# Optimization experiments

Hardware: AMD Instinct MI355X
Metric: run time of the kernel (lower is better)

## Reference

```python
import jax, jax.numpy as jnp
import numpy as np

H = 8
D_MODEL = 1024
D_K = D_MODEL // H
NEG = -1000000000.0


def layer_norm(x, a, b, eps=1e-06):
    # torch std: unbiased (ddof=1); module divides by (std + eps)
    mean = jnp.mean(x, axis=-1, keepdims=True)
    var = jnp.sum((x - mean) ** 2, axis=-1, keepdims=True) / (x.shape[-1] - 1)
    std = jnp.sqrt(var)
    return a * (x - mean) / (std + eps) + b


def setup_inputs() -> dict:
    key = jax.random.key(0)
    ks = jax.random.split(key, 12)
    B, S, D = 8, 1024, D_MODEL
    inp = {
        "query": jax.random.normal(ks[0], (B, S, D), jnp.float32),
        "value": jax.random.normal(ks[1], (B, S, D), jnp.float32),
        "key": jax.random.normal(ks[2], (B, S, D), jnp.float32),
        "mask": jax.random.randint(ks[3], (B, S), 0, 2, jnp.int32),
        "ln_a": jnp.ones((D,), jnp.float32),
        "ln_b": jnp.zeros((D,), jnp.float32),
        "wq": jax.random.normal(ks[4], (D, D), jnp.float32) * 0.02,
        "bq": jnp.zeros((D,), jnp.float32),
        "wk": jax.random.normal(ks[5], (D, D), jnp.float32) * 0.02,
        "bk": jnp.zeros((D,), jnp.float32),
        "wv": jax.random.normal(ks[6], (D, D), jnp.float32) * 0.02,
        "bv": jnp.zeros((D,), jnp.float32),
        "w_aoa": jax.random.normal(ks[7], (2 * D, 2 * D), jnp.float32) * 0.02,  # [out, in]
        "b_aoa": jnp.zeros((2 * D,), jnp.float32),
    }
    return inp


def reference(query, value, key, mask, ln_a, ln_b, wq, bq, wk, bk, wv, bv, w_aoa, b_aoa):
    B, S, D = query.shape
    # mask [B,S] -> [B,1,1,S]
    m = mask[:, None, None, :]
    # norm_q
    q = layer_norm(query, ln_a, ln_b)
    # QKV projections, split heads -> [B,H,S,Dk]
    def split_heads(x):
        return x.reshape(B, -1, H, D_K).transpose(0, 2, 1, 3)
    q_ = split_heads(q @ wq.T + bq)
    k_ = split_heads(key @ wk.T + bk)
    v_ = split_heads(value @ wv.T + bv)
    scores = jnp.einsum("bhqd,bhkd->bhqk", q_, k_) / jnp.sqrt(jnp.float32(D_K))
    scores = jnp.where(m == 0, NEG, scores)
    p = jax.nn.softmax(scores, axis=-1)
    x = jnp.einsum("bhqk,bhkd->bhqd", p, v_)
    x = x.transpose(0, 2, 1, 3).reshape(B, S, D)
    # AoA: concat with (normed) query, linear to 2D, GLU
    z = jnp.concatenate([x, q], axis=-1) @ w_aoa.T + b_aoa
    a, g = jnp.split(z, 2, axis=-1)
    return a * jax.nn.sigmoid(g)
```

## Files before the change

kernel.cpp:

```cpp
#include <hip/hip_runtime.h>

typedef __attribute__((ext_vector_type(8))) __bf16 bf16x8;
typedef __attribute__((ext_vector_type(4))) float f32x4;
typedef __attribute__((ext_vector_type(16))) float f32x16;
typedef __attribute__((ext_vector_type(2))) int i32x2;

__device__ __forceinline__ ushort f2b(float f) {
    uint u = __builtin_bit_cast(uint, f);
    u += 0x7fffu + ((u >> 16) & 1u);
    return (ushort)(u >> 16);
}
__device__ __forceinline__ float b2f(ushort h) {
    uint u = ((uint)h) << 16;
    return __builtin_bit_cast(float, u);
}
__device__ __forceinline__ uint cvtpk(float a, float b) {
    uint r;
    asm("v_cvt_pk_bf16_f32 %0, %1, %2" : "=v"(r) : "v"(a), "v"(b));
    return r;
}

__global__ __launch_bounds__(256) void cast_all(const float* __restrict__ wq,
                                                const float* __restrict__ wk,
                                                const float* __restrict__ wv,
                                                const float* __restrict__ waoa,
                                                ushort* __restrict__ wqb,
                                                ushort* __restrict__ wab) {
    int bid = blockIdx.x;
    int tid = threadIdx.x;
    if (bid < 3072) {
        const float* src = (bid < 1024) ? wq : ((bid < 2048) ? wk : wv);
        float4 v = *(const float4*)(src + ((size_t)(bid & 1023) * 256 + tid) * 4);
        ushort4 o;
        o.x = f2b(v.x); o.y = f2b(v.y); o.z = f2b(v.z); o.w = f2b(v.w);
        *(ushort4*)(wqb + (size_t)bid * 1024 + tid * 4) = o;
    } else {
        int b3 = bid - 3072;
        int n1 = b3 >> 1;
        int c = (b3 & 1) * 1024 + tid * 4;
        int q = ((n1 & 63) | ((n1 >> 7) << 6)) + ((n1 >> 6) & 1) * 1024;
        float4 v = *(const float4*)(waoa + (size_t)q * 2048 + c);
        ushort4 o;
        o.x = f2b(v.x); o.y = f2b(v.y); o.z = f2b(v.z); o.w = f2b(v.w);
        *(ushort4*)(wab + (size_t)n1 * 2048 + c) = o;
    }
}

__global__ __launch_bounds__(256) void ln_kernel(const float* __restrict__ x,
                                                 const float* __restrict__ ga,
                                                 const float* __restrict__ be,
                                                 ushort* __restrict__ xq) {
    const int row = blockIdx.x, tid = threadIdx.x;
    __shared__ float red[4];
    float4 v = ((const float4*)(x + (size_t)row * 1024))[tid];
    float sm = v.x + v.y + v.z + v.w;
    for (int off = 32; off; off >>= 1) sm += __shfl_xor(sm, off);
    if ((tid & 63) == 0) red[tid >> 6] = sm;
    __syncthreads();
    float mean = (red[0] + red[1] + red[2] + red[3]) * (1.f / 1024.f);
    __syncthreads();
    float dx = v.x - mean, dy = v.y - mean, dz = v.z - mean, dw = v.w - mean;
    float s2 = dx * dx + dy * dy + dz * dz + dw * dw;
    for (int off = 32; off; off >>= 1) s2 += __shfl_xor(s2, off);
    if ((tid & 63) == 0) red[tid >> 6] = s2;
    __syncthreads();
    float var = (red[0] + red[1] + red[2] + red[3]) * (1.f / 1023.f);
    float inv = 1.f / (sqrtf(var) + 1e-6f);
    float4 g = ((const float4*)ga)[tid];
    float4 bb = ((const float4*)be)[tid];
    ushort4 o;
    o.x = f2b(g.x * dx * inv + bb.x);
    o.y = f2b(g.y * dy * inv + bb.y);
    o.z = f2b(g.z * dz * inv + bb.z);
    o.w = f2b(g.w * dw * inv + bb.w);
    *(ushort4*)&xq[(size_t)row * 2048 + 1024 + tid * 4] = o;
}

template <int MODE>
__global__ __launch_bounds__(512, 2) void gemm6(const ushort* __restrict__ Aq, int ldaq,
                                                const ushort* __restrict__ B, int ldb,
                                                const float* __restrict__ bias0,
                                                void* __restrict__ out0,
                                                int K, int NB) {
    __shared__ ushort lds[2][32768];

    const int tid = threadIdx.x;
    const int w = tid >> 6, l = tid & 63;
    const int wr = w >> 2, wcn = w & 3;
    const int r16 = l & 15, g4 = l >> 4;

    const int bid = blockIdx.x;
    const int cpx = gridDim.x >> 3;
    const int swz = (bid & 7) * cpx + (bid >> 3);
    const int m0 = (swz / NB) * 256;
    const int n0 = (swz % NB) * 256;

    const ushort* A = Aq;
    const int lda = ldaq;

    const int srow8 = l >> 3;
    const int sxor8 = ((l & 7) ^ srow8) * 8;
    const ushort* As0 = A + (size_t)(m0 + w * 8 + srow8) * lda + sxor8;
    const ushort* Bs0 = B + (size_t)(n0 + w * 8 + srow8) * ldb + sxor8;

    f32x4 acc[8][4];
#pragma unroll
    for (int i = 0; i < 8; i++)
#pragma unroll
        for (int j = 0; j < 4; j++) acc[i][j] = (f32x4){0.f, 0.f, 0.f, 0.f};

    const int sw16 = (r16 & 7) << 4;
    char* ldsb = (char*)&lds[0][0];

#define STAGE_H(sel_, HS_, kt_)                                                            \
    do {                                                                                   \
        const int mat_ = (HS_)&1, half_ = (HS_) >> 1;                                      \
        const ushort* sb_ = mat_ ? Bs0 : As0;                                              \
        const int ld_ = mat_ ? ldb : lda;                                                  \
        _Pragma("unroll") for (int li_ = 0; li_ < 2; li_++) {                              \
            const ushort* src_ = sb_ + (size_t)(half_ * 128 + li_ * 64) * ld_ + (kt_)*64;  \
            int dst_ = (sel_)*65536 + mat_ * 32768 + half_ * 16384 + li_ * 8192 + w * 1024;\
            __builtin_amdgcn_global_load_lds(                                              \
                (const __attribute__((address_space(1))) void*)src_,                       \
                (__attribute__((address_space(3))) void*)(ldsb + dst_), 16, 0, 0);         \
        }                                                                                  \
    } while (0)

    auto LDA4 = [&](bf16x8 (&dst)[4][2], int sel, int half) {
#pragma unroll
        for (int ai = 0; ai < 4; ai++)
#pragma unroll
            for (int ks = 0; ks < 2; ks++)
                dst[ai][ks] = *(const bf16x8*)(ldsb + sel * 65536 + half * 16384 +
                                               (wr * 16 + 32 * ai + r16) * 128 +
                                               ((ks * 64 + g4 * 16) ^ sw16));
    };
    auto LDB2 = [&](bf16x8 (&dst)[2][2], int sel, int half) {
#pragma unroll
        for (int bi = 0; bi < 2; bi++)
#pragma unroll
            for (int ks = 0; ks < 2; ks++)
                dst[bi][ks] = *(const bf16x8*)(ldsb + sel * 65536 + 32768 + half * 16384 +
                                               (wcn * 16 + 64 * bi + r16) * 128 +
                                               ((ks * 64 + g4 * 16) ^ sw16));
    };
    auto MM = [&](bf16x8 (&af)[4][2], bf16x8 (&bf)[2][2], int A0, int B0) {
        __builtin_amdgcn_s_setprio(1);
#pragma unroll
        for (int ks = 0; ks < 2; ks++)
#pragma unroll
            for (int ai = 0; ai < 4; ai++)
#pragma unroll
                for (int bi = 0; bi < 2; bi++)
                    acc[A0 + ai][B0 + bi] = __builtin_amdgcn_mfma_f32_16x16x32_bf16(
                        af[ai][ks], bf[bi][ks], acc[A0 + ai][B0 + bi], 0, 0, 0);
        __builtin_amdgcn_s_setprio(0);
    };

    const int NT = K >> 6;

    STAGE_H(0, 0, 0); STAGE_H(0, 1, 0); STAGE_H(0, 2, 0); STAGE_H(0, 3, 0);
    STAGE_H(1, 0, 1); STAGE_H(1, 1, 1); STAGE_H(1, 2, 1);
    asm volatile("s_waitcnt vmcnt(10)" ::: "memory");
    __builtin_amdgcn_s_barrier();

    bf16x8 aL[4][2], aH[4][2], bL[2][2], bH[2][2];

    for (int t = 0; t < NT - 2; ++t) {
        const int sel = t & 1;
        LDA4(aL, sel, 0); LDB2(bL, sel, 0);
        STAGE_H(sel ^ 1, 3, t + 1);
        __builtin_amdgcn_s_barrier();
        MM(aL, bL, 0, 0);
        asm volatile("s_waitcnt vmcnt(10)" ::: "memory");
        __builtin_amdgcn_s_barrier();
        LDA4(aH, sel, 1);
        STAGE_H(sel, 0, t + 2);
        __builtin_amdgcn_s_barrier();
        MM(aH, bL, 4, 0);
        asm volatile("s_waitcnt vmcnt(10)" ::: "memory");
        __builtin_amdgcn_s_barrier();
        LDB2(bH, sel, 1);
        STAGE_H(sel, 1, t + 2);
        __builtin_amdgcn_s_barrier();
        MM(aH, bH, 4, 2);
        __builtin_amdgcn_s_barrier();
        STAGE_H(sel, 2, t + 2);
        __builtin_amdgcn_s_barrier();
        MM(aL, bH, 0, 2);
        asm volatile("s_waitcnt vmcnt(10)" ::: "memory");
        __builtin_amdgcn_s_barrier();
    }
    {
        const int sel = (NT - 2) & 1;
        LDA4(aL, sel, 0); LDB2(bL, sel, 0);
        STAGE_H(sel ^ 1, 3, NT - 1);
        __builtin_amdgcn_s_barrier();
        MM(aL, bL, 0, 0);
        asm volatile("s_waitcnt vmcnt(10)" ::: "memory");
        __builtin_amdgcn_s_barrier();
        LDA4(aH, sel, 1);
        __builtin_amdgcn_s_barrier();
        MM(aH, bL, 4, 0);
        asm volatile("s_waitcnt vmcnt(8)" ::: "memory");
        __builtin_amdgcn_s_barrier();
        LDB2(bH, sel, 1);
        __builtin_amdgcn_s_barrier();
        MM(aH, bH, 4, 2);
        __builtin_amdgcn_s_barrier();
        MM(aL, bH, 0, 2);
        asm volatile("s_waitcnt vmcnt(4)" ::: "memory");
        __builtin_amdgcn_s_barrier();
    }
    {
        const int sel = (NT - 1) & 1;
        LDA4(aL, sel, 0); LDB2(bL, sel, 0);
        __builtin_amdgcn_s_barrier();
        MM(aL, bL, 0, 0);
        asm volatile("s_waitcnt vmcnt(2)" ::: "memory");
        __builtin_amdgcn_s_barrier();
        LDA4(aH, sel, 1);
        __builtin_amdgcn_s_barrier();
        MM(aH, bL, 4, 0);
        asm volatile("s_waitcnt vmcnt(0)" ::: "memory");
        __builtin_amdgcn_s_barrier();
        LDB2(bH, sel, 1);
        MM(aH, bH, 4, 2);
        MM(aL, bH, 0, 2);
    }
#undef STAGE_H

    float* out = (float*)out0;
#pragma unroll
    for (int bp = 0; bp < 2; bp++) {
        int j = (n0 >> 1) + wcn * 16 + 64 * bp + r16;
        float bsa = bias0[j];
        float bsg = bias0[j + 1024];
#pragma unroll
        for (int a_ = 0; a_ < 8; a_++) {
            int mr = m0 + wr * 16 + 32 * a_ + g4 * 4;
#pragma unroll
            for (int r = 0; r < 4; r++) {
                float av = acc[a_][2 * bp][r] + bsa;
                float gv = acc[a_][2 * bp + 1][r] + bsg;
                out[(size_t)(mr + r) * 1024 + j] = av * (1.f / (1.f + __expf(-gv)));
            }
        }
    }
}

__global__ __launch_bounds__(512, 2) void gemm7q(const ushort* __restrict__ A, int lda,
                                                 const ushort* __restrict__ B, int ldb,
                                                 const float* __restrict__ bias,
                                                 ushort* __restrict__ C, float qscale) {
    __shared__ ushort lds[2][24576];

    const int tid = threadIdx.x;
    const int w = tid >> 6, l = tid & 63;
    const int wr = w >> 2, wcn = w & 3;
    const int r16 = l & 15, g4 = l >> 4;

    const int bid = blockIdx.x;
    const int cpx = gridDim.x >> 3;
    const int swz = (bid & 7) * cpx + (bid >> 3);
    const int m0 = (swz >> 2) * 128;
    const int n0 = (swz & 3) * 256;

    const int srow8 = l >> 3;
    const int sxor8 = ((l & 7) ^ srow8) * 8;
    const ushort* As0 = A + (size_t)(m0 + w * 8 + srow8) * lda + sxor8;
    const ushort* Bs0 = B + (size_t)(n0 + w * 8 + srow8) * ldb + sxor8;

    f32x4 acc[4][4];
#pragma unroll
    for (int i = 0; i < 4; i++)
#pragma unroll
        for (int j = 0; j < 4; j++) acc[i][j] = (f32x4){0.f, 0.f, 0.f, 0.f};

    const int sw16 = (r16 & 7) << 4;
    char* ldsb = (char*)&lds[0][0];

#define STAGE_A(sel_, h_, kt_)                                                             \
    __builtin_amdgcn_global_load_lds(                                                      \
        (const __attribute__((address_space(1))) void*)(As0 + (size_t)((h_)*64) * lda + (kt_)*64), \
        (__attribute__((address_space(3))) void*)(ldsb + (sel_)*49152 + (h_)*8192 + w * 1024), 16, 0, 0)
#define STAGE_B(sel_, h_, li_, kt_)                                                        \
    __builtin_amdgcn_global_load_lds(                                                      \
        (const __attribute__((address_space(1))) void*)(Bs0 + (size_t)((h_)*128 + (li_)*64) * ldb + (kt_)*64), \
        (__attribute__((address_space(3))) void*)(ldsb + (sel_)*49152 + 16384 + (h_)*16384 + (li_)*8192 + w * 1024), 16, 0, 0)

    auto LDA2 = [&](bf16x8 (&dst)[2][2], int sel, int half) {
#pragma unroll
        for (int ai = 0; ai < 2; ai++)
#pragma unroll
            for (int ks = 0; ks < 2; ks++)
                dst[ai][ks] = *(const bf16x8*)(ldsb + sel * 49152 + half * 8192 +
                                               (wr * 16 + 32 * ai + r16) * 128 +
                                               ((ks * 64 + g4 * 16) ^ sw16));
    };
    auto LDB2 = [&](bf16x8 (&dst)[2][2], int sel, int half) {
#pragma unroll
        for (int bi = 0; bi < 2; bi++)
#pragma unroll
            for (int ks = 0; ks < 2; ks++)
                dst[bi][ks] = *(const bf16x8*)(ldsb + sel * 49152 + 16384 + half * 16384 +
                                               (wcn * 16 + 64 * bi + r16) * 128 +
                                               ((ks * 64 + g4 * 16) ^ sw16));
    };
    auto MM = [&](bf16x8 (&af)[2][2], bf16x8 (&bf)[2][2], int A0, int B0) {
        __builtin_amdgcn_s_setprio(1);
#pragma unroll
        for (int ks = 0; ks < 2; ks++)
#pragma unroll
            for (int ai = 0; ai < 2; ai++)
#pragma unroll
                for (int bi = 0; bi < 2; bi++)
                    acc[A0 + ai][B0 + bi] = __builtin_amdgcn_mfma_f32_16x16x32_bf16(
                        af[ai][ks], bf[bi][ks], acc[A0 + ai][B0 + bi], 0, 0, 0);
        __builtin_amdgcn_s_setprio(0);
    };

    const int NT = 16;

    STAGE_A(0, 0, 0); STAGE_B(0, 0, 0, 0); STAGE_B(0, 0, 1, 0);
    STAGE_A(0, 1, 0); STAGE_B(0, 1, 0, 0); STAGE_B(0, 1, 1, 0);
    STAGE_A(1, 0, 1); STAGE_B(1, 0, 0, 1); STAGE_B(1, 0, 1, 1);
    STAGE_A(1, 1, 1);
    asm volatile("s_waitcnt vmcnt(7)" ::: "memory");
    __builtin_amdgcn_s_barrier();

    bf16x8 aL[2][2], aH[2][2], bL[2][2], bH[2][2];

    for (int t = 0; t < NT - 2; ++t) {
        const int sel = t & 1;
        LDA2(aL, sel, 0); LDB2(bL, sel, 0);
        STAGE_B(sel ^ 1, 1, 0, t + 1); STAGE_B(sel ^ 1, 1, 1, t + 1);
        __builtin_amdgcn_s_barrier();
        MM(aL, bL, 0, 0);
        asm volatile("s_waitcnt vmcnt(8)" ::: "memory");
        __builtin_amdgcn_s_barrier();
        LDA2(aH, sel, 1);
        STAGE_A(sel, 0, t + 2);
        __builtin_amdgcn_s_barrier();
        MM(aH, bL, 2, 0);
        asm volatile("s_waitcnt vmcnt(7)" ::: "memory");
        __builtin_amdgcn_s_barrier();
        LDB2(bH, sel, 1);
        STAGE_B(sel, 0, 0, t + 2); STAGE_B(sel, 0, 1, t + 2);
        __builtin_amdgcn_s_barrier();
        MM(aH, bH, 2, 2);
        __builtin_amdgcn_s_barrier();
        STAGE_A(sel, 1, t + 2);
        __builtin_amdgcn_s_barrier();
        MM(aL, bH, 0, 2);
        asm volatile("s_waitcnt vmcnt(7)" ::: "memory");
        __builtin_amdgcn_s_barrier();
    }
    {
        const int sel = (NT - 2) & 1;
        LDA2(aL, sel, 0); LDB2(bL, sel, 0);
        STAGE_B(sel ^ 1, 1, 0, NT - 1); STAGE_B(sel ^ 1, 1, 1, NT - 1);
        __builtin_amdgcn_s_barrier();
        MM(aL, bL, 0, 0);
        asm volatile("s_waitcnt vmcnt(8)" ::: "memory");
        __builtin_amdgcn_s_barrier();
        LDA2(aH, sel, 1);
        __builtin_amdgcn_s_barrier();
        MM(aH, bL, 2, 0);
        asm volatile("s_waitcnt vmcnt(6)" ::: "memory");
        __builtin_amdgcn_s_barrier();
        LDB2(bH, sel, 1);
        __builtin_amdgcn_s_barrier();
        MM(aH, bH, 2, 2);
        __builtin_amdgcn_s_barrier();
        MM(aL, bH, 0, 2);
        asm volatile("s_waitcnt vmcnt(3)" ::: "memory");
        __builtin_amdgcn_s_barrier();
    }
    {
        const int sel = (NT - 1) & 1;
        LDA2(aL, sel, 0); LDB2(bL, sel, 0);
        __builtin_amdgcn_s_barrier();
        MM(aL, bL, 0, 0);
        asm volatile("s_waitcnt vmcnt(2)" ::: "memory");
        __builtin_amdgcn_s_barrier();
        LDA2(aH, sel, 1);
        __builtin_amdgcn_s_barrier();
        MM(aH, bL, 2, 0);
        asm volatile("s_waitcnt vmcnt(0)" ::: "memory");
        __builtin_amdgcn_s_barrier();
        LDB2(bH, sel, 1);
        MM(aH, bH, 2, 2);
        MM(aL, bH, 0, 2);
    }
#undef STAGE_A
#undef STAGE_B

#pragma unroll
    for (int b_ = 0; b_ < 4; b_++) {
        int n = n0 + wcn * 16 + 64 * b_ + r16;
        float bs = bias[n];
#pragma unroll
        for (int a_ = 0; a_ < 4; a_++) {
            int mr = m0 + wr * 16 + 32 * a_ + g4 * 4;
#pragma unroll
            for (int r = 0; r < 4; r++)
                C[(size_t)(mr + r) * 1024 + n] = f2b((acc[a_][b_][r] + bs) * qscale);
        }
    }
}

__global__ __launch_bounds__(512, 2) void gemm7kv(const float* __restrict__ Akf,
                                                  const float* __restrict__ Avf,
                                                  const ushort* __restrict__ B, int ldb,
                                                  const float* __restrict__ biask,
                                                  const float* __restrict__ biasv,
                                                  ushort* __restrict__ Kb,
                                                  ushort* __restrict__ Vt) {
    __shared__ ushort lds[2][24576];

    const int tid = threadIdx.x;
    const int w = tid >> 6, l = tid & 63;
    const int wr = w >> 2, wcn = w & 3;
    const int r16 = l & 15, g4 = l >> 4;

    const int bid = blockIdx.x;
    const int cpx = gridDim.x >> 3;
    const int swz = (bid & 7) * cpx + (bid >> 3);
    const int m0 = (swz >> 3) * 128;
    const int n0 = (swz & 7) * 256;
    const int kreg = n0 >> 10;
    const float* Af = kreg ? Avf : Akf;

    const int srow8 = l >> 3;
    const int sxor8 = ((l & 7) ^ srow8) * 8;
    const ushort* Bs0 = B + (size_t)(n0 + w * 8 + srow8) * ldb + sxor8;

    const int arow = w * 8 + srow8;
    const float* As0 = Af + (size_t)(m0 + arow) * 1024 + (l & 7) * 8;
    const int awr = arow * 128 + (((l & 7) * 16) ^ ((arow & 7) << 4));

    f32x4 acc[4][4];
#pragma unroll
    for (int i = 0; i < 4; i++)
#pragma unroll
        for (int j = 0; j < 4; j++) acc[i][j] = (f32x4){0.f, 0.f, 0.f, 0.f};

    const int sw16 = (r16 & 7) << 4;
    char* ldsb = (char*)&lds[0][0];

#define STAGE_B(sel_, h_, li_, kt_)                                                        \
    __builtin_amdgcn_global_load_lds(                                                      \
        (const __attribute__((address_space(1))) void*)(Bs0 + (size_t)((h_)*128 + (li_)*64) * ldb + (kt_)*64), \
        (__attribute__((address_space(3))) void*)(ldsb + (sel_)*49152 + 16384 + (h_)*16384 + (li_)*8192 + w * 1024), 16, 0, 0)

    float4 ah[2][2];
    auto GL4 = [&](float4& d, const float* p) {
        asm volatile("global_load_dwordx4 %0, %1, off" : "=&v"(d) : "v"(p) : "memory");
    };
    auto LOAD_A = [&](int kt) {
#pragma unroll
        for (int h = 0; h < 2; h++) {
            const float* p = As0 + (size_t)h * 64 * 1024 + kt * 64;
            GL4(ah[h][0], p);
            GL4(ah[h][1], p + 4);
        }
    };
    auto WRITE_A = [&](int sel) {
#pragma unroll
        for (int h = 0; h < 2; h++) {
            union { bf16x8 v; uint u[4]; } pk;
            pk.u[0] = cvtpk(ah[h][0].x, ah[h][0].y);
            pk.u[1] = cvtpk(ah[h][0].z, ah[h][0].w);
            pk.u[2] = cvtpk(ah[h][1].x, ah[h][1].y);
            pk.u[3] = cvtpk(ah[h][1].z, ah[h][1].w);
            *(bf16x8*)(ldsb + sel * 49152 + h * 8192 + awr) = pk.v;
        }
    };

    auto LDA2 = [&](bf16x8 (&dst)[2][2], int sel, int half) {
#pragma unroll
        for (int ai = 0; ai < 2; ai++)
#pragma unroll
            for (int ks = 0; ks < 2; ks++)
                dst[ai][ks] = *(const bf16x8*)(ldsb + sel * 49152 + half * 8192 +
                                               (wr * 16 + 32 * ai + r16) * 128 +
                                               ((ks * 64 + g4 * 16) ^ sw16));
    };
    auto LDB2 = [&](bf16x8 (&dst)[2][2], int sel, int half) {
#pragma unroll
        for (int bi = 0; bi < 2; bi++)
#pragma unroll
            for (int ks = 0; ks < 2; ks++)
                dst[bi][ks] = *(const bf16x8*)(ldsb + sel * 49152 + 16384 + half * 16384 +
                                               (wcn * 16 + 64 * bi + r16) * 128 +
                                               ((ks * 64 + g4 * 16) ^ sw16));
    };
    auto MM = [&](bf16x8 (&af)[2][2], bf16x8 (&bf)[2][2], int A0, int B0) {
        __builtin_amdgcn_s_setprio(1);
#pragma unroll
        for (int ks = 0; ks < 2; ks++)
#pragma unroll
            for (int ai = 0; ai < 2; ai++)
#pragma unroll
                for (int bi = 0; bi < 2; bi++)
                    acc[A0 + ai][B0 + bi] = __builtin_amdgcn_mfma_f32_16x16x32_bf16(
                        af[ai][ks], bf[bi][ks], acc[A0 + ai][B0 + bi], 0, 0, 0);
        __builtin_amdgcn_s_setprio(0);
    };

    const int NT = 16;

    STAGE_B(0, 0, 0, 0); STAGE_B(0, 0, 1, 0);
    LOAD_A(0);
    STAGE_B(0, 1, 0, 0); STAGE_B(0, 1, 1, 0);
    asm volatile("s_waitcnt vmcnt(2)" ::: "memory");
    __builtin_amdgcn_sched_barrier(0);
    WRITE_A(0);
    asm volatile("s_waitcnt lgkmcnt(0)" ::: "memory");
    __builtin_amdgcn_sched_barrier(0);
    __builtin_amdgcn_s_barrier();

    bf16x8 aL[2][2], aH[2][2], bL[2][2], bH[2][2];

    for (int t = 0; t < NT; ++t) {
        const int sel = t & 1;
        const bool pf = (t + 1 < NT);
        LDA2(aL, sel, 0); LDB2(bL, sel, 0);
        if (pf) {
            STAGE_B(sel ^ 1, 0, 0, t + 1); STAGE_B(sel ^ 1, 0, 1, t + 1);
            LOAD_A(t + 1);
        }
        __builtin_amdgcn_s_barrier();
        MM(aL, bL, 0, 0);
        __builtin_amdgcn_s_barrier();
        LDA2(aH, sel, 1);
        __builtin_amdgcn_s_barrier();
        MM(aH, bL, 2, 0);
        if (pf) asm volatile("s_waitcnt vmcnt(6)" ::: "memory");
        else    asm volatile("s_waitcnt vmcnt(0)" ::: "memory");
        __builtin_amdgcn_s_barrier();
        LDB2(bH, sel, 1);
        if (pf) { STAGE_B(sel ^ 1, 1, 0, t + 1); STAGE_B(sel ^ 1, 1, 1, t + 1); }
        __builtin_amdgcn_s_barrier();
        MM(aH, bH, 2, 2);
        __builtin_amdgcn_s_barrier();
        if (pf) {
            asm volatile("s_waitcnt vmcnt(2)" ::: "memory");
            __builtin_amdgcn_sched_barrier(0);
            WRITE_A(sel ^ 1);
            asm volatile("s_waitcnt lgkmcnt(0)" ::: "memory");
            __builtin_amdgcn_sched_barrier(0);
        }
        __builtin_amdgcn_s_barrier();
        MM(aL, bH, 0, 2);
        __builtin_amdgcn_s_barrier();
    }
#undef STAGE_B

    const int nr0 = n0 & 1023;
    const float* bias = kreg ? biasv : biask;
    if (kreg == 0) {
#pragma unroll
        for (int b_ = 0; b_ < 4; b_++) {
            int n = nr0 + wcn * 16 + 64 * b_ + r16;
            float bs = bias[n];
#pragma unroll
            for (int a_ = 0; a_ < 4; a_++) {
                int mr = m0 + wr * 16 + 32 * a_ + g4 * 4;
#pragma unroll
                for (int r = 0; r < 4; r++)
                    Kb[(size_t)(mr + r) * 1024 + n] = f2b(acc[a_][b_][r] + bs);
            }
        }
    } else {
#pragma unroll
        for (int b_ = 0; b_ < 4; b_++) {
            int n = nr0 + wcn * 16 + 64 * b_ + r16;
            float bs = bias[n];
            int h = n >> 7, d = n & 127;
#pragma unroll
            for (int a_ = 0; a_ < 4; a_++) {
                int mr = m0 + wr * 16 + 32 * a_ + g4 * 4;
                int bb = mr >> 10, s_ = mr & 1023;
                ushort4 o;
                o.x = f2b(acc[a_][b_][0] + bs);
                o.y = f2b(acc[a_][b_][1] + bs);
                o.z = f2b(acc[a_][b_][2] + bs);
                o.w = f2b(acc[a_][b_][3] + bs);
                *(ushort4*)&Vt[((size_t)(bb * 8 + h) * 128 + d) * 1024 + s_] = o;
            }
        }
    }
}

__global__ __launch_bounds__(256, 2) void attn_kernel(const ushort* __restrict__ Q,
                                                      const ushort* __restrict__ Kt,
                                                      const ushort* __restrict__ Vt,
                                                      const int* __restrict__ mask,
                                                      ushort* __restrict__ xq) {
    __shared__ ushort Ks[2][8192];
    __shared__ ushort Vs[2][8192];

    const int tid = threadIdx.x;
    const int l = tid & 63, wid = tid >> 6;
    const int ql = l & 31, hi = l >> 5;
    const int id = blockIdx.x;
    const int bh = ((id >> 6) << 3) | (id & 7);
    const int qb = (id >> 3) & 7;
    const int b = bh >> 3, h = bh & 7;
    const int q0 = qb * 128 + wid * 32;

    bf16x8 qf[8];
    const ushort* Qrow = Q + (size_t)(b * 1024 + q0 + ql) * 1024 + h * 128 + hi * 8;
#pragma unroll
    for (int ks = 0; ks < 8; ks++) qf[ks] = *(const bf16x8*)(Qrow + ks * 16);

    const ushort* Kg = Kt + ((size_t)b * 1024) * 1024 + h * 128;
    const ushort* Vg = Vt + (size_t)(b * 8 + h) * 128 * 1024;
    const int* mptr = mask + b * 1024;

    f32x16 xacc[4];
#pragma unroll
    for (int i = 0; i < 4; i++)
#pragma unroll
        for (int r = 0; r < 16; r++) xacc[i][r] = 0.f;
    float mrow = -INFINITY, lrow = 0.f, sclp = 0.f;
    bool resc = true;
    bf16x8 pa[4];

    auto STAGE_K = [&](int sel, int t) {
        const int kv0 = t * 64;
#pragma unroll
        for (int it = 0; it < 4; ++it) {
            int ob = it * 4096 + wid * 1024;
            int o = ob + l * 16;
            int row = o >> 8;
            int sc = (o & 255) ^ ((row & 7) << 4);
            const ushort* src = Kg + (size_t)(kv0 + row) * 1024 + (sc >> 1);
            __builtin_amdgcn_global_load_lds((const __attribute__((address_space(1))) void*)src,
                (__attribute__((address_space(3))) void*)((char*)&Ks[sel][0] + ob), 16, 0, 0);
        }
    };
    auto STAGE_V = [&](int sel, int t) {
        const int kv0 = t * 64;
#pragma unroll
        for (int it = 0; it < 4; ++it) {
            int ob = it * 4096 + wid * 1024;
            int o = ob + l * 16;
            int d = o >> 7;
            int sc = (o & 127) ^ ((d & 7) << 4);
            const ushort* src = Vg + (size_t)d * 1024 + kv0 + (sc >> 1);
            __builtin_amdgcn_global_load_lds((const __attribute__((address_space(1))) void*)src,
                (__attribute__((address_space(3))) void*)((char*)&Vs[sel][0] + ob), 16, 0, 0);
        }
    };

    auto QK = [&](f32x16 (&s)[2], int sel, unsigned long long wt) {
        const char* Kb_ = (const char*)&Ks[sel][0];
#pragma unroll
        for (int sub = 0; sub < 2; sub++) {
            f32x16 sa, sb;
#pragma unroll
            for (int r = 0; r < 16; r++) { sa[r] = 0.f; sb[r] = 0.f; }
            const int rowk = sub * 32 + ql;
            const char* kr = Kb_ + rowk * 256;
            const int sw = (rowk & 7) << 4;
            __builtin_amdgcn_s_setprio(1);
#pragma unroll
            for (int ks = 0; ks < 4; ks++) {
                bf16x8 k0 = *(const bf16x8*)(kr + (((2 * ks) * 32 + hi * 16) ^ sw));
                bf16x8 k1 = *(const bf16x8*)(kr + (((2 * ks + 1) * 32 + hi * 16) ^ sw));
                sa = __builtin_amdgcn_mfma_f32_32x32x16_bf16(k0, qf[2 * ks], sa, 0, 0, 0);
                sb = __builtin_amdgcn_mfma_f32_32x32x16_bf16(k1, qf[2 * ks + 1], sb, 0, 0, 0);
            }
            __builtin_amdgcn_s_setprio(0);
#pragma unroll
            for (int r = 0; r < 16; r++) sa[r] += sb[r];
#pragma unroll
            for (int q2 = 0; q2 < 4; q2++) {
                uint nib = (uint)(wt >> (8 * q2 + 4 * hi + 32 * sub)) & 15u;
#pragma unroll
                for (int r = 0; r < 4; r++)
                    if (!((nib >> r) & 1u)) sa[4 * q2 + r] = -1e9f;
            }
            s[sub] = sa;
        }
    };
    auto PV = [&](int sel) {
        const char* Vb_ = (const char*)&Vs[sel][0];
        if (resc) {
#pragma unroll
            for (int df = 0; df < 4; df++)
#pragma unroll
                for (int r = 0; r < 16; r++) xacc[df][r] *= sclp;
        }
        __builtin_amdgcn_s_setprio(1);
#pragma unroll
        for (int ks2 = 0; ks2 < 4; ks2++) {
#pragma unroll
            for (int df = 0; df < 4; df++) {
                const int d = df * 32 + ql;
                bf16x8 vfr = *(const bf16x8*)(Vb_ + d * 128 + ((ks2 * 32 + hi * 16) ^ ((d & 7) << 4)));
                xacc[df] = __builtin_amdgcn_mfma_f32_32x32x16_bf16(vfr, pa[ks2], xacc[df], 0, 0, 0);
            }
        }
        __builtin_amdgcn_s_setprio(0);
    };
    auto SOFTMAX = [&](f32x16 (&s)[2]) {
        float v[16];
#pragma unroll
        for (int r = 0; r < 16; r++) v[r] = fmaxf(s[0][r], s[1][r]);
#pragma unroll
        for (int st = 8; st; st >>= 1)
#pragma unroll
            for (int i = 0; i < 8; i++)
                if (i < st) v[i] = fmaxf(v[i], v[i + st]);
        float pmax = fmaxf(v[0], __shfl_xor(v[0], 32));
        if (!__all(pmax - mrow <= 8.f)) {
            float mn = fmaxf(mrow, pmax);
            sclp = __expf(mrow - mn);
            mrow = mn;
            resc = true;
        } else {
            resc = false;
        }
        float rsum = 0.f;
#pragma unroll
        for (int res = 0; res < 2; res++)
#pragma unroll
            for (int r = 0; r < 16; r++) {
                float p = __expf(s[res][r] - mrow);
                s[res][r] = p;
                rsum += p;
            }
        rsum += __shfl_xor(rsum, 32);
        lrow = (resc ? lrow * sclp : lrow) + rsum;
#pragma unroll
        for (int sub = 0; sub < 2; sub++)
#pragma unroll
            for (int g = 0; g < 2; g++) {
                const int b0 = g * 8;
                uint lo01 = cvtpk(s[sub][b0 + 0], s[sub][b0 + 1]);
                uint lo23 = cvtpk(s[sub][b0 + 2], s[sub][b0 + 3]);
                uint hi01 = cvtpk(s[sub][b0 + 4], s[sub][b0 + 5]);
                uint hi23 = cvtpk(s[sub][b0 + 6], s[sub][b0 + 7]);
                i32x2 r02 = __builtin_amdgcn_permlane32_swap((int)lo01, (int)hi01, false, false);
                i32x2 r13 = __builtin_amdgcn_permlane32_swap((int)lo23, (int)hi23, false, false);
                union { bf16x8 vv; uint u[4]; } pk;
                pk.u[0] = (uint)r02.x;
                pk.u[1] = (uint)r13.x;
                pk.u[2] = (uint)r02.y;
                pk.u[3] = (uint)r13.y;
                pa[sub * 2 + g] = pk.vv;
            }
    };

    STAGE_K(0, 0);
    int mv = mptr[l];
    asm volatile("s_waitcnt vmcnt(0)" ::: "memory");
    __syncthreads();
    STAGE_K(1, 1);
    STAGE_V(0, 0);
    unsigned long long wt = __ballot(mv != 0);
    mv = mptr[64 + l];
    f32x16 s[2];
    QK(s, 0, wt);
    SOFTMAX(s);
    int kc = 1, vc = 0;

    for (int u = 1; u < 16; ++u) {
        wt = __ballot(mv != 0);
        asm volatile("s_waitcnt vmcnt(0)" ::: "memory");
        __syncthreads();
        if (u < 15) STAGE_K(kc ^ 1, u + 1);
        STAGE_V(vc ^ 1, u);
        if (u < 15) mv = mptr[(u + 1) * 64 + l];

        QK(s, kc, wt);
        PV(vc);
        SOFTMAX(s);

        kc ^= 1; vc ^= 1;
    }

    asm volatile("s_waitcnt vmcnt(0)" ::: "memory");
    __syncthreads();
    PV(vc);

    const float inv = 1.f / lrow;
    const size_t orow = (size_t)(b * 1024 + q0 + ql) * 2048 + h * 128;
#pragma unroll
    for (int df = 0; df < 4; df++) {
#pragma unroll
        for (int q2 = 0; q2 < 4; q2++) {
            ushort4 o;
            o.x = f2b(xacc[df][4 * q2 + 0] * inv);
            o.y = f2b(xacc[df][4 * q2 + 1] * inv);
            o.z = f2b(xacc[df][4 * q2 + 2] * inv);
            o.w = f2b(xacc[df][4 * q2 + 3] * inv);
            *(ushort4*)&xq[orow + df * 32 + 8 * q2 + 4 * hi] = o;
        }
    }
}

extern "C" void kernel_launch(void* const* d_in, const int* in_sizes, int n_in,
                              void* d_out, int out_size, void* d_ws, size_t ws_size,
                              hipStream_t stream) {
    const float* query = (const float*)d_in[0];
    const float* value = (const float*)d_in[1];
    const float* key   = (const float*)d_in[2];
    const int*   mask  = (const int*)d_in[3];
    const float* ln_a  = (const float*)d_in[4];
    const float* ln_b  = (const float*)d_in[5];
    const float* wq    = (const float*)d_in[6];
    const float* bq    = (const float*)d_in[7];
    const float* wk    = (const float*)d_in[8];
    const float* bk    = (const float*)d_in[9];
    const float* wv    = (const float*)d_in[10];
    const float* bv    = (const float*)d_in[11];
    const float* waoa  = (const float*)d_in[12];
    const float* baoa  = (const float*)d_in[13];
    float* out = (float*)d_out;

    char* w8 = (char*)d_ws;
    ushort* xq   = (ushort*)(w8);
    ushort* Qb   = (ushort*)(w8 + 33554432);
    ushort* Kb   = (ushort*)(w8 + 50331648);
    ushort* Vt   = (ushort*)(w8 + 67108864);
    ushort* wqb  = (ushort*)(w8 + 117440512);
    ushort* wab  = (ushort*)(w8 + 123731968);

    cast_all<<<7168, 256, 0, stream>>>(wq, wk, wv, waoa, wqb, wab);
    ln_kernel<<<8192, 256, 0, stream>>>(query, ln_a, ln_b, xq);

    const float qscale = 0.08838834764831845f;

    gemm7q<<<256, 512, 0, stream>>>(xq + 1024, 2048, wqb, 1024, bq, Qb, qscale);
    gemm7kv<<<512, 512, 0, stream>>>(key, value, wqb + 1048576, 1024, bk, bv, Kb, Vt);

    attn_kernel<<<512, 256, 0, stream>>>(Qb, Kb, Vt, mask, xq);

    gemm6<1><<<256, 512, 0, stream>>>(xq, 2048, wab, 2048, baoa, out, 2048, 8);
}
```

Baseline: 216.2 us.

## Pre-cast key/value to bf16 and stage A via direct LDS loads with deeper pipeline

Key and value activations are now cast to bf16 in the cast_all kernel, and gemm7kv loads A tiles straight into LDS with global_load_lds instead of a register round-trip plus conversion. The main loop is restructured into a two-stage-ahead prefetch with explicit epilogue iterations. This removes per-iteration conversion and register pressure in the GEMM. The cost is an extra pass that reads 64MB of fp32 and writes 32MB of bf16 through the cast kernel.

Measured after the change: 227.5 us. 1.05x slower.

```diff
diff --git a/kernel.cpp b/kernel.cpp
--- a/kernel.cpp
+++ b/kernel.cpp
@@ -20,22 +20,32 @@
     return r;
 }
 
-__global__ __launch_bounds__(256) void cast_all(const float* __restrict__ wq,
+__global__ __launch_bounds__(256) void cast_all(const float* __restrict__ key,
+                                                const float* __restrict__ value,
+                                                const float* __restrict__ wq,
                                                 const float* __restrict__ wk,
                                                 const float* __restrict__ wv,
                                                 const float* __restrict__ waoa,
+                                                ushort* __restrict__ keyb,
                                                 ushort* __restrict__ wqb,
                                                 ushort* __restrict__ wab) {
     int bid = blockIdx.x;
     int tid = threadIdx.x;
-    if (bid < 3072) {
-        const float* src = (bid < 1024) ? wq : ((bid < 2048) ? wk : wv);
-        float4 v = *(const float4*)(src + ((size_t)(bid & 1023) * 256 + tid) * 4);
+    if (bid < 16384) {
+        const float* src = (bid < 8192) ? key : value;
+        float4 v = *(const float4*)(src + ((size_t)(bid & 8191) * 256 + tid) * 4);
         ushort4 o;
         o.x = f2b(v.x); o.y = f2b(v.y); o.z = f2b(v.z); o.w = f2b(v.w);
-        *(ushort4*)(wqb + (size_t)bid * 1024 + tid * 4) = o;
+        *(ushort4*)(keyb + (size_t)bid * 1024 + tid * 4) = o;
+    } else if (bid < 19456) {
+        int b2 = bid - 16384;
+        const float* src = (b2 < 1024) ? wq : ((b2 < 2048) ? wk : wv);
+        float4 v = *(const float4*)(src + ((size_t)(b2 & 1023) * 256 + tid) * 4);
+        ushort4 o;
+        o.x = f2b(v.x); o.y = f2b(v.y); o.z = f2b(v.z); o.w = f2b(v.w);
+        *(ushort4*)(wqb + (size_t)b2 * 1024 + tid * 4) = o;
     } else {
-        int b3 = bid - 3072;
+        int b3 = bid - 19456;
         int n1 = b3 >> 1;
         int c = (b3 & 1) * 1024 + tid * 4;
         int q = ((n1 & 63) | ((n1 >> 7) << 6)) + ((n1 >> 6) & 1) * 1024;
@@ -410,8 +420,8 @@
     }
 }
 
-__global__ __launch_bounds__(512, 2) void gemm7kv(const float* __restrict__ Akf,
-                                                  const float* __restrict__ Avf,
+__global__ __launch_bounds__(512, 2) void gemm7kv(const ushort* __restrict__ Ak,
+                                                  const ushort* __restrict__ Av,
                                                   const ushort* __restrict__ B, int ldb,
                                                   const float* __restrict__ biask,
                                                   const float* __restrict__ biasv,
@@ -430,15 +440,13 @@
     const int m0 = (swz >> 3) * 128;
     const int n0 = (swz & 7) * 256;
     const int kreg = n0 >> 10;
-    const float* Af = kreg ? Avf : Akf;
+    const ushort* A = kreg ? Av : Ak;
+    const int lda = 1024;
 
     const int srow8 = l >> 3;
     const int sxor8 = ((l & 7) ^ srow8) * 8;
+    const ushort* As0 = A + (size_t)(m0 + w * 8 + srow8) * lda + sxor8;
     const ushort* Bs0 = B + (size_t)(n0 + w * 8 + srow8) * ldb + sxor8;
-
-    const int arow = w * 8 + srow8;
-    const float* As0 = Af + (size_t)(m0 + arow) * 1024 + (l & 7) * 8;
-    const int awr = arow * 128 + (((l & 7) * 16) ^ ((arow & 7) << 4));
 
     f32x4 acc[4][4];
 #pragma unroll
@@ -449,35 +457,15 @@
     const int sw16 = (r16 & 7) << 4;
     char* ldsb = (char*)&lds[0][0];
 
+#define STAGE_A(sel_, h_, kt_)                                                             \
+    __builtin_amdgcn_global_load_lds(                                                      \
+        (const __attribute__((address_space(1))) void*)(As0 + (size_t)((h_)*64) * lda + (kt_)*64), \
+        (__attribute__((address_space(3))) void*)(ldsb + (sel_)*49152 + (h_)*8192 + w * 1024), 16, 0, 0)
 #define STAGE_B(sel_, h_, li_, kt_)                                                        \
     __builtin_amdgcn_global_load_lds(                                                      \
         (const __attribute__((address_space(1))) void*)(Bs0 + (size_t)((h_)*128 + (li_)*64) * ldb + (kt_)*64), \
         (__attribute__((address_space(3))) void*)(ldsb + (sel_)*49152 + 16384 + (h_)*16384 + (li_)*8192 + w * 1024), 16, 0, 0)
 
-    float4 ah[2][2];
-    auto GL4 = [&](float4& d, const float* p) {
-        asm volatile("global_load_dwordx4 %0, %1, off" : "=&v"(d) : "v"(p) : "memory");
-    };
-    auto LOAD_A = [&](int kt) {
-#pragma unroll
-        for (int h = 0; h < 2; h++) {
-            const float* p = As0 + (size_t)h * 64 * 1024 + kt * 64;
-            GL4(ah[h][0], p);
-            GL4(ah[h][1], p + 4);
-        }
-    };
-    auto WRITE_A = [&](int sel) {
-#pragma unroll
-        for (int h = 0; h < 2; h++) {
-            union { bf16x8 v; uint u[4]; } pk;
-            pk.u[0] = cvtpk(ah[h][0].x, ah[h][0].y);
-            pk.u[1] = cvtpk(ah[h][0].z, ah[h][0].w);
-            pk.u[2] = cvtpk(ah[h][1].x, ah[h][1].y);
-            pk.u[3] = cvtpk(ah[h][1].z, ah[h][1].w);
-            *(bf16x8*)(ldsb + sel * 49152 + h * 8192 + awr) = pk.v;
-        }
-    };
-
     auto LDA2 = [&](bf16x8 (&dst)[2][2], int sel, int half) {
 #pragma unroll
         for (int ai = 0; ai < 2; ai++)
@@ -511,51 +499,78 @@
 
     const int NT = 16;
 
-    STAGE_B(0, 0, 0, 0); STAGE_B(0, 0, 1, 0);
-    LOAD_A(0);
-    STAGE_B(0, 1, 0, 0); STAGE_B(0, 1, 1, 0);
-    asm volatile("s_waitcnt vmcnt(2)" ::: "memory");
-    __builtin_amdgcn_sched_barrier(0);
-    WRITE_A(0);
-    asm volatile("s_waitcnt lgkmcnt(0)" ::: "memory");
-    __builtin_amdgcn_sched_barrier(0);
+    STAGE_A(0, 0, 0); STAGE_B(0, 0, 0, 0); STAGE_B(0, 0, 1, 0);
+    STAGE_A(0, 1, 0); STAGE_B(0, 1, 0, 0); STAGE_B(0, 1, 1, 0);
+    STAGE_A(1, 0, 1); STAGE_B(1, 0, 0, 1); STAGE_B(1, 0, 1, 1);
+    STAGE_A(1, 1, 1);
+    asm volatile("s_waitcnt vmcnt(7)" ::: "memory");
     __builtin_amdgcn_s_barrier();
 
     bf16x8 aL[2][2], aH[2][2], bL[2][2], bH[2][2];
 
-    for (int t = 0; t < NT; ++t) {
+    for (int t = 0; t < NT - 2; ++t) {
         const int sel = t & 1;
-        const bool pf = (t + 1 < NT);
         LDA2(aL, sel, 0); LDB2(bL, sel, 0);
-        if (pf) {
-            STAGE_B(sel ^ 1, 0, 0, t + 1); STAGE_B(sel ^ 1, 0, 1, t + 1);
-            LOAD_A(t + 1);
-        }
+        STAGE_B(sel ^ 1, 1, 0, t + 1); STAGE_B(sel ^ 1, 1, 1, t + 1);
         __builtin_amdgcn_s_barrier();
         MM(aL, bL, 0, 0);
+        asm volatile("s_waitcnt vmcnt(8)" ::: "memory");
         __builtin_amdgcn_s_barrier();
         LDA2(aH, sel, 1);
+        STAGE_A(sel, 0, t + 2);
         __builtin_amdgcn_s_barrier();
         MM(aH, bL, 2, 0);
-        if (pf) asm volatile("s_waitcnt vmcnt(6)" ::: "memory");
-        else    asm volatile("s_waitcnt vmcnt(0)" ::: "memory");
+        asm volatile("s_waitcnt vmcnt(7)" ::: "memory");
         __builtin_amdgcn_s_barrier();
         LDB2(bH, sel, 1);
-        if (pf) { STAGE_B(sel ^ 1, 1, 0, t + 1); STAGE_B(sel ^ 1, 1, 1, t + 1); }
+        STAGE_B(sel, 0, 0, t + 2); STAGE_B(sel, 0, 1, t + 2);
         __builtin_amdgcn_s_barrier();
         MM(aH, bH, 2, 2);
         __builtin_amdgcn_s_barrier();
-        if (pf) {
-            asm volatile("s_waitcnt vmcnt(2)" ::: "memory");
-            __builtin_amdgcn_sched_barrier(0);
-            WRITE_A(sel ^ 1);
-            asm volatile("s_waitcnt lgkmcnt(0)" ::: "memory");
-            __builtin_amdgcn_sched_barrier(0);
-        }
+        STAGE_A(sel, 1, t + 2);
         __builtin_amdgcn_s_barrier();
         MM(aL, bH, 0, 2);
-        __builtin_amdgcn_s_barrier();
-    }
+        asm volatile("s_waitcnt vmcnt(7)" ::: "memory");
+        __builtin_amdgcn_s_barrier();
+    }
+    {
+        const int sel = (NT - 2) & 1;
+        LDA2(aL, sel, 0); LDB2(bL, sel, 0);
+        STAGE_B(sel ^ 1, 1, 0, NT - 1); STAGE_B(sel ^ 1, 1, 1, NT - 1);
+        __builtin_amdgcn_s_barrier();
+        MM(aL, bL, 0, 0);
+        asm volatile("s_waitcnt vmcnt(8)" ::: "memory");
+        __builtin_amdgcn_s_barrier();
+        LDA2(aH, sel, 1);
+        __builtin_amdgcn_s_barrier();
+        MM(aH, bL, 2, 0);
+        asm volatile("s_waitcnt vmcnt(6)" ::: "memory");
+        __builtin_amdgcn_s_barrier();
+        LDB2(bH, sel, 1);
+        __builtin_amdgcn_s_barrier();
+        MM(aH, bH, 2, 2);
+        __builtin_amdgcn_s_barrier();
+        MM(aL, bH, 0, 2);
+        asm volatile("s_waitcnt vmcnt(3)" ::: "memory");
+        __builtin_amdgcn_s_barrier();
+    }
+    {
+        const int sel = (NT - 1) & 1;
+        LDA2(aL, sel, 0); LDB2(bL, sel, 0);
+        __builtin_amdgcn_s_barrier();
+        MM(aL, bL, 0, 0);
+        asm volatile("s_waitcnt vmcnt(2)" ::: "memory");
+        __builtin_amdgcn_s_barrier();
+        LDA2(aH, sel, 1);
+        __builtin_amdgcn_s_barrier();
+        MM(aH, bL, 2, 0);
+        asm volatile("s_waitcnt vmcnt(0)" ::: "memory");
+        __builtin_amdgcn_s_barrier();
+        LDB2(bH, sel, 1);
+        MM(aH, bH, 2, 2);
+        MM(aL, bH, 0, 2);
+    }
+#undef STAGE_A
 #undef STAGE_B
 
     const int nr0 = n0 & 1023;
@@ -828,16 +843,18 @@
     ushort* Qb   = (ushort*)(w8 + 33554432);
     ushort* Kb   = (ushort*)(w8 + 50331648);
     ushort* Vt   = (ushort*)(w8 + 67108864);
+    ushort* keyb = (ushort*)(w8 + 83886080);
     ushort* wqb  = (ushort*)(w8 + 117440512);
     ushort* wab  = (ushort*)(w8 + 123731968);
 
-    cast_all<<<7168, 256, 0, stream>>>(wq, wk, wv, waoa, wqb, wab);
+    cast_all<<<23552, 256, 0, stream>>>(key, value, wq, wk, wv, waoa, keyb, wqb, wab);
     ln_kernel<<<8192, 256, 0, stream>>>(query, ln_a, ln_b, xq);
 
     const float qscale = 0.08838834764831845f;
+    ushort* valb = keyb + 8388608;
 
     gemm7q<<<256, 512, 0, stream>>>(xq + 1024, 2048, wqb, 1024, bq, Qb, qscale);
-    gemm7kv<<<512, 512, 0, stream>>>(key, value, wqb + 1048576, 1024, bk, bv, Kb, Vt);
+    gemm7kv<<<512, 512, 0, stream>>>(keyb, valb, wqb + 1048576, 1024, bk, bv, Kb, Vt);
 
     attn_kernel<<<512, 256, 0, stream>>>(Qb, Kb, Vt, mask, xq);
 
```
